# Kernel tuning notes

Measured on AMD Instinct MI355X. Metric: run time of the kernel, lower is better.

The kernel has to match this reference:

```python
import jax, jax.numpy as jnp
import numpy as np

V = 5000      # output_class_dim
E = 512       # embed_dim
F = 512       # 2 * listener_hidden_dim
H = 512       # speller_hidden_dim
HEADS = 4
HD = F // HEADS  # 128
STEPS = 64    # max_label_len
B, T = 32, 1024


def setup_inputs() -> dict:
    key = jax.random.key(0)
    ks = jax.random.split(key, 10)
    s = 0.05
    return {
        "listener_feature": jax.random.normal(ks[0], (B, T, F), jnp.float32),
        "embedding": jax.random.normal(ks[1], (V, E), jnp.float32) * s,
        # LSTM cell (single layer, torch gate order i,f,g,o)
        "W_ih": jax.random.normal(ks[2], (4 * H, E + F), jnp.float32) * s,
        "W_hh": jax.random.normal(ks[3], (4 * H, H), jnp.float32) * s,
        "b_ih": jax.random.normal(ks[4], (4 * H,), jnp.float32) * s,
        "b_hh": jax.random.normal(ks[5], (4 * H,), jnp.float32) * s,
        # predict_hid: Linear(2H -> 512)
        "Wp": jax.random.normal(ks[6], (512, 2 * H), jnp.float32) * s,
        "bp": jax.random.normal(ks[7], (512,), jnp.float32) * s,
        # character_distribution: Linear(512 -> V)
        "Wc": jax.random.normal(ks[8], (V, 512), jnp.float32) * s,
        "bc": jax.random.normal(ks[9], (V,), jnp.float32) * s,
    }


def _decode(listener_feature, embedding, W_ih, W_hh, b_ih, b_hh, Wp, bp, Wc, bc):
    b = listener_feature.shape[0]
    lf_heads = listener_feature.reshape(b, T, HEADS, HD)  # [B,T,h,d]

    def lstm_cell(x, h, c):
        gates = x @ W_ih.T + h @ W_hh.T + (b_ih + b_hh)
        i, f, g, o = jnp.split(gates, 4, axis=-1)
        c_new = jax.nn.sigmoid(f) * c + jax.nn.sigmoid(i) * jnp.tanh(g)
        h_new = jax.nn.sigmoid(o) * jnp.tanh(c_new)
        return h_new, c_new

    def step(carry, _):
        h, c, rnn_in = carry
        h, c = lstm_cell(rnn_in, h, c)                       # rnn_output = h [B,H]
        ds = h.reshape(b, HEADS, HD)                          # decoder state per head
        energy = jnp.einsum('bhd,bthd->bht', ds, lf_heads)    # dot attention
        scores = jax.nn.softmax(energy, axis=-1)              # [B,h,T]
        context = jnp.einsum('bht,bthd->bhd', scores, lf_heads).reshape(b, F)
        concat = jnp.concatenate([h, context], axis=-1)       # [B,2H]
        hid = jnp.maximum(concat @ Wp.T + bp, 0.0)            # ReLU MLP
        raw_pred = jax.nn.log_softmax(hid @ Wc.T + bc, axis=-1)
        # greedy feedback (teacher_force_rate = 0 since ground_truth is None)
        tok = jnp.argmax(raw_pred, axis=-1)                   # [B]
        rnn_in_next = jnp.concatenate([embedding[tok], context], axis=-1)
        return (h, c, rnn_in_next), (raw_pred, scores[:, -1, :])

    h0 = jnp.zeros((b, H), listener_feature.dtype)
    c0 = jnp.zeros((b, H), listener_feature.dtype)
    # initial input: embedding of token 0, concat first listener frame
    emb0 = jnp.broadcast_to(embedding[0], (b, E))
    rnn_in0 = jnp.concatenate([emb0, listener_feature[:, 0, :]], axis=-1)

    _, (raw_pred_seq, attn_seq) = jax.lax.scan(step, (h0, c0, rnn_in0), None, length=STEPS)
    return raw_pred_seq, attn_seq  # [S,B,V], [S,B,T] (last head, as in original)


def reference(listener_feature, embedding, W_ih, W_hh, b_ih, b_hh, Wp, bp, Wc, bc):
    return _decode(listener_feature, embedding, W_ih, W_hh, b_ih, b_hh, Wp, bp, Wc, bc)
```

## Files before the change

### kernel.cpp

```cpp
#include <hip/hip_runtime.h>
#include <math.h>
#include <stdint.h>


#define NB 512
#define NT 256

constexpr int Tv = 1024, Vv = 5000, STEPS = 64;

constexpr int MCNT = 0;
constexpr int GEN  = 16;
constexpr int GCNT = 64;
constexpr int GFLG = 1024;
constexpr int ACNT = 2048;
constexpr int LCNT = 2560;
constexpr int WSU  = 4096;

constexpr int XH   = 0;
constexpr int HB   = XH + 32*1024;
constexpr int HID  = HB + 2*32*512;
constexpr int PART = HID + 32*512;
constexpr int E3   = PART + 32*4*16*130;
constexpr int PM   = E3 + 32*1024;
constexpr int PSUM = PM + 32*256;
constexpr int PIDX = PSUM + 32*256;
constexpr int MLS  = PIDX + 32*256;

__device__ __forceinline__ float sigm(float x) { return 1.f / (1.f + expf(-x)); }

__device__ __forceinline__ float ld4(const float* p) {
  return __hip_atomic_load(const_cast<float*>(p), __ATOMIC_RELAXED, __HIP_MEMORY_SCOPE_AGENT);
}
__device__ __forceinline__ void st4(float* p, float v) {
  __hip_atomic_store(p, v, __ATOMIC_RELAXED, __HIP_MEMORY_SCOPE_AGENT);
}
__device__ __forceinline__ float2 ld8(const float* p) {
  unsigned long long u = __hip_atomic_load(
      reinterpret_cast<unsigned long long*>(const_cast<float*>(p)),
      __ATOMIC_RELAXED, __HIP_MEMORY_SCOPE_AGENT);
  union { unsigned long long u; float2 f; } c; c.u = u; return c.f;
}
__device__ __forceinline__ void st8(float* p, float2 v) {
  union { float2 f; unsigned long long u; } c; c.f = v;
  __hip_atomic_store(reinterpret_cast<unsigned long long*>(p), c.u,
                     __ATOMIC_RELAXED, __HIP_MEMORY_SCOPE_AGENT);
}
__device__ __forceinline__ int ld4i(const int* p) {
  return (int)__hip_atomic_load(reinterpret_cast<unsigned*>(const_cast<int*>(p)),
                                __ATOMIC_RELAXED, __HIP_MEMORY_SCOPE_AGENT);
}
__device__ __forceinline__ void st4i(int* p, int v) {
  __hip_atomic_store(reinterpret_cast<unsigned*>(p), (unsigned)v,
                     __ATOMIC_RELAXED, __HIP_MEMORY_SCOPE_AGENT);
}
__device__ __forceinline__ unsigned ld_rlx(unsigned* p) {
  return __hip_atomic_load(p, __ATOMIC_RELAXED, __HIP_MEMORY_SCOPE_AGENT);
}
__device__ __forceinline__ void st_rlx(unsigned* p, unsigned v) {
  __hip_atomic_store(p, v, __ATOMIC_RELAXED, __HIP_MEMORY_SCOPE_AGENT);
}
__device__ __forceinline__ unsigned add_rlx(unsigned* p, unsigned v) {
  return __hip_atomic_fetch_add(p, v, __ATOMIC_RELAXED, __HIP_MEMORY_SCOPE_AGENT);
}

__device__ __forceinline__ void gsync(unsigned* wsu, int blk, int tid, unsigned& myGen) {
  __syncthreads();
  if (tid == 0) {
    const unsigned target = ++myGen;
    const int grp = blk >> 4;
    unsigned o = add_rlx(&wsu[GCNT + grp*16], 1u);
    if (o == target*16u - 1u) {
      unsigned o2 = add_rlx(&wsu[MCNT], 1u);
      if (o2 == target*32u - 1u) st_rlx(&wsu[GEN], target);
    }
    if ((blk & 15) == 0) {
      while (ld_rlx(&wsu[GEN]) != target) __builtin_amdgcn_s_sleep(2);
      st_rlx(&wsu[GFLG + grp*32], target);
    } else {
      while (ld_rlx(&wsu[GFLG + grp*32]) != target) __builtin_amdgcn_s_sleep(2);
    }
  }
  __syncthreads();
}

__global__ void speller_init(const float* __restrict__ LF, const float* __restrict__ Emb,
                             float* __restrict__ wsf, unsigned* __restrict__ wsu) {
  int b = blockIdx.x;
  for (int i = threadIdx.x; i < 512; i += NT) {
    st4(wsf + XH + b*1024 + i,       Emb[i]);
    st4(wsf + XH + b*1024 + 512 + i, LF[(size_t)b*Tv*512 + i]);
    st4(wsf + HB + b*512 + i,        0.f);
  }
  if (b == 0) for (int i = threadIdx.x; i < WSU; i += NT) st_rlx(wsu + i, 0u);
}

struct LdsA { float Wg[8][1536]; float gb[8]; };
struct LdsB { float Wc[20][512]; float Wp[2][1024]; float bcl[20]; float bpl[2]; };
union  LdsU { LdsA a; LdsB b; };

__device__ __forceinline__ void gate_accum_A(float acc[8][2], const float* __restrict__ wsf,
                                             const float (&Wg)[8][1536],
                                             int ks, int b0, int hbuf) {
#pragma unroll 2
  for (int q = 0; q < 8; ++q) {
    const int k4 = 512 + (q*16 + ks)*4;
    float2 xa[2], xb[2];
#pragma unroll
    for (int i = 0; i < 2; ++i) {
      const float* p = wsf + XH + (size_t)(b0+i)*1024 + k4;
      xa[i] = ld8(p); xb[i] = ld8(p + 2);
    }
#pragma unroll
    for (int r = 0; r < 8; ++r) {
      float4 wv = *(const float4*)(&Wg[r][k4]);
#pragma unroll
      for (int i = 0; i < 2; ++i)
        acc[r][i] += wv.x*xa[i].x + wv.y*xa[i].y + wv.z*xb[i].x + wv.w*xb[i].y;
    }
  }
#pragma unroll 2
  for (int q = 0; q < 8; ++q) {
    const int k4 = (q*16 + ks)*4;
    float2 xa[2], xb[2];
#pragma unroll
    for (int i = 0; i < 2; ++i) {
      const float* p = wsf + HB + hbuf*16384 + (size_t)(b0+i)*512 + k4;
      xa[i] = ld8(p); xb[i] = ld8(p + 2);
    }
#pragma unroll
    for (int r = 0; r < 8; ++r) {
      float4 wv = *(const float4*)(&Wg[r][1024 + k4]);
#pragma unroll
      for (int i = 0; i < 2; ++i)
        acc[r][i] += wv.x*xa[i].x + wv.y*xa[i].y + wv.z*xb[i].x + wv.w*xb[i].y;
    }
  }
}

__launch_bounds__(NT, 2)
__global__ void speller_main(const float* __restrict__ LF, const float* __restrict__ Emb,
                             const float* __restrict__ Wih, const float* __restrict__ Whh,
                             const float* __restrict__ bih, const float* __restrict__ bhh,
                             const float* __restrict__ Wp,  const float* __restrict__ bp,
                             const float* __restrict__ Wc,  const float* __restrict__ bc,
                             float* __restrict__ out, unsigned* __restrict__ wsu,
                             float* __restrict__ wsf) {
  const int blk = blockIdx.x, tid = threadIdx.x;
  unsigned myGen = 0;
  __shared__ LdsU lds;
  __shared__ float scr[784];
  __shared__ int  sint[300];

  const int ab = blk >> 4, atc = blk & 15;
  const int aw = tid >> 6, aln = tid & 63;

  float4 lfr[32];
  {
    const float4* src = (const float4*)(LF +
        (((size_t)ab*Tv + atc*64 + aln)*512 + aw*128));
#pragma unroll
    for (int q = 0; q < 32; ++q) lfr[q] = src[q];
  }

  if (blk < 256) {
    const int u0 = blk * 2;
    for (int idx = tid; idx < 8*1536; idx += NT) {
      int r = idx / 1536, k = idx - r*1536;
      int g = r >> 1, uu = r & 1;
      int row = g*512 + u0 + uu;
      lds.a.Wg[r][k] = (k < 1024) ? Wih[(size_t)row*1024 + k]
                                  : Whh[(size_t)row*512 + (k-1024)];
    }
    if (tid < 8) {
      int g = tid >> 1, uu = tid & 1, row = g*512 + u0 + uu;
      lds.a.gb[tid] = bih[row] + bhh[row];
    }
  } else {
    const int blk2 = blk - 256, v0 = blk2*20, rp0 = blk2*2;
    if (v0 < Vv) {
      for (int idx = tid; idx < 20*512; idx += NT) {
        int vi = idx >> 9, k = idx & 511;
        lds.b.Wc[vi][k] = Wc[(size_t)(v0+vi)*512 + k];
      }
      if (tid < 20) lds.b.bcl[tid] = bc[v0+tid];
    }
    for (int idx = tid; idx < 2048; idx += NT) {
      int r = idx >> 10, k = idx & 1023;
      lds.b.Wp[r][k] = Wp[(size_t)(rp0+r)*1024 + k];
    }
    if (tid < 2) lds.b.bpl[tid] = bp[rp0+tid];
  }
  __syncthreads();

  float acc[8][2];
  float c_reg[2][2];
#pragma unroll
  for (int uu = 0; uu < 2; ++uu)
#pragma unroll
    for (int i = 0; i < 2; ++i) c_reg[uu][i] = 0.f;
  float lgv[20];

  if (blk < 256) {
    const int ks = tid & 15, b0 = (tid >> 4) * 2;
#pragma unroll
    for (int r = 0; r < 8; ++r)
#pragma unroll
      for (int i = 0; i < 2; ++i) acc[r][i] = 0.f;
    gate_accum_A(acc, wsf, lds.a.Wg, ks, b0, 0);
  }

#pragma unroll 1
  for (int s = 0; s < STEPS; ++s) {
    const int wbuf = (s + 1) & 1;

    if (blk < 256) {
      const int u0 = blk * 2;
      const int ks = tid & 15, b0 = (tid >> 4) * 2;
#pragma unroll 2
      for (int q = 0; q < 8; ++q) {
        const int k4 = (q*16 + ks)*4;
        float2 xa[2], xb[2];
#pragma unroll
        for (int i = 0; i < 2; ++i) {
          const float* p = wsf + XH + (size_t)(b0+i)*1024 + k4;
          xa[i] = ld8(p); xb[i] = ld8(p + 2);
        }
#pragma unroll
        for (int r = 0; r < 8; ++r) {
          float4 wv = *(const float4*)(&lds.a.Wg[r][k4]);
#pragma unroll
          for (int i = 0; i < 2; ++i)
            acc[r][i] += wv.x*xa[i].x + wv.y*xa[i].y + wv.z*xb[i].x + wv.w*xb[i].y;
        }
      }
#pragma unroll
      for (int r = 0; r < 8; ++r)
#pragma unroll
        for (int i = 0; i < 2; ++i) {
          float v = acc[r][i];
          v += __shfl_xor(v, 8); v += __shfl_xor(v, 4);
          v += __shfl_xor(v, 2); v += __shfl_xor(v, 1);
          acc[r][i] = v + lds.a.gb[r];
        }
      float hnew[2][2];
#pragma unroll
      for (int uu = 0; uu < 2; ++uu)
#pragma unroll
        for (int i = 0; i < 2; ++i) {
          float cn = sigm(acc[2+uu][i]) * c_reg[uu][i]
                   + sigm(acc[uu][i]) * tanhf(acc[4+uu][i]);
          c_reg[uu][i] = cn;
          hnew[uu][i] = sigm(acc[6+uu][i]) * tanhf(cn);
        }
      if (ks == 0) {
#pragma unroll
        for (int i = 0; i < 2; ++i)
          st8(wsf + HB + wbuf*16384 + (size_t)(b0+i)*512 + u0,
              make_float2(hnew[0][i], hnew[1][i]));
      }
    } else if (s > 0) {
      const int blk2 = blk - 256;
      if (blk2 < 250) {
        const int v0 = blk2 * 20, bb = tid >> 3, ks = tid & 7;
        if (ks == 0) {
          float2 ml = ld8(wsf + MLS + 2*bb);
          float sub = ml.x + ml.y;
#pragma unroll
          for (int vi = 0; vi < 20; ++vi)
            out[(size_t)(s-1)*160000 + (size_t)bb*5000 + v0 + vi] = lgv[vi] - sub;
        }
      }
    }
    gsync(wsu, blk, tid, myGen);

    {
      float* hs = scr;
      {
        float2 hv = ld8(wsf + HB + wbuf*16384 + (size_t)ab*512 + tid*2);
        hs[tid*2] = hv.x; hs[tid*2+1] = hv.y;
      }
      __syncthreads();
      float e = 0.f;
      {
        const float4* hp = (const float4*)(hs + aw*128);
#pragma unroll
        for (int q = 0; q < 32; ++q) {
          float4 f = lfr[q], hh = hp[q];
          e += f.x*hh.x + f.y*hh.y + f.z*hh.z + f.w*hh.w;
        }
      }
      float m = e;
#pragma unroll
      for (int off = 32; off; off >>= 1) m = fmaxf(m, __shfl_xor(m, off));
      float p = expf(e - m);
      float l = p;
#pragma unroll
      for (int off = 32; off; off >>= 1) l += __shfl_xor(l, off);
      if (aw == 3) st4(wsf + E3 + (size_t)ab*1024 + atc*64 + aln, e);
      float* pr = wsf + PART + (size_t)((ab*4 + aw)*16 + atc)*130;
#pragma unroll
      for (int ch = 0; ch < 2; ++ch) {
        float c[64];
#pragma unroll
        for (int q = 0; q < 16; ++q) {
          float4 f = lfr[ch*16 + q];
          c[4*q+0] = p*f.x; c[4*q+1] = p*f.y; c[4*q+2] = p*f.z; c[4*q+3] = p*f.w;
        }
#pragma unroll
        for (int o = 32; o >= 1; o >>= 1) {
#pragma unroll
          for (int j = 0; j < 32; ++j) {
            if (j < o) {
              float keep = (aln & o) ? c[j + o] : c[j];
              float send = (aln & o) ? c[j] : c[j + o];
              c[j] = keep + __shfl_xor(send, o);
            }
          }
        }
        st4(pr + 2 + ch*64 + aln, c[0]);
      }
      if (aln == 0) st8(pr, make_float2(m, l));
      __syncthreads();
      if (tid == 0) {
        unsigned old = add_rlx(&wsu[ACNT + ab*16], 1u);
        sint[0] = (old == (unsigned)(s*16 + 15));
      }
      __syncthreads();
      if (sint[0]) {
        const int w2 = tid >> 6, ln2 = tid & 63;
        const float* pb = wsf + PART + (size_t)(ab*4 + w2)*16*130;
        float M = -1e30f;
        float mv[16], lv[16];
#pragma unroll
        for (int i = 0; i < 16; ++i) { float2 t = ld8(pb + i*130); mv[i] = t.x; lv[i] = t.y; M = fmaxf(M, t.x); }
        float L = 0.f;
        float sc[16];
#pragma unroll
        for (int i = 0; i < 16; ++i) { sc[i] = expf(mv[i] - M); L += lv[i] * sc[i]; }
        float cc0 = 0.f, cc1 = 0.f;
#pragma unroll
        for (int i = 0; i < 16; ++i) {
          float2 cx = ld8(pb + i*130 + 2 + 2*ln2);
          cc0 += sc[i]*cx.x; cc1 += sc[i]*cx.y;
        }
        float invL = 1.f / L;
        st8(wsf + XH + (size_t)ab*1024 + 512 + w2*128 + 2*ln2,
            make_float2(cc0*invL, cc1*invL));
        if (ln2 == 0) { scr[768 + w2*2] = M; scr[769 + w2*2] = L; }
        __syncthreads();
        float M3 = scr[768 + 6], iL3 = 1.f / scr[768 + 7];
        for (int i = tid; i < 1024; i += NT)
          out[(size_t)10240000 + ((size_t)(s*32 + ab))*1024 + i] =
              expf(ld4(wsf + E3 + (size_t)ab*1024 + i) - M3) * iL3;
      }
    }
    gsync(wsu, blk, tid, myGen);

    if (blk >= 256) {
      const int blk2 = blk - 256, rp0 = blk2*2;
      const int bb = tid & 31, ks = tid >> 5;
      const float* xr = (ks < 4) ? (wsf + HB + wbuf*16384 + (size_t)bb*512 + ks*128)
                                 : (wsf + XH + (size_t)bb*1024 + (ks-4)*128 + 512);
      const int kb = ks * 128;
      const float4* w0 = (const float4*)(&lds.b.Wp[0][kb]);
      const float4* w1 = (const float4*)(&lds.b.Wp[1][kb]);
      float a0 = 0.f, a1 = 0.f;
#pragma unroll 8
      for (int q = 0; q < 32; ++q) {
        float2 xva = ld8(xr + q*4), xvb = ld8(xr + q*4 + 2);
        float4 wv0 = w0[q], wv1 = w1[q];
        a0 += wv0.x*xva.x + wv0.y*xva.y + wv0.z*xvb.x + wv0.w*xvb.y;
        a1 += wv1.x*xva.x + wv1.y*xva.y + wv1.z*xvb.x + wv1.w*xvb.y;
      }
      scr[ks*32 + bb] = a0; scr[256 + ks*32 + bb] = a1;
      __syncthreads();
      if (tid < 64) {
        int r = tid >> 5, b2 = tid & 31;
        float ssum = 0.f;
#pragma unroll
        for (int j = 0; j < 8; ++j) ssum += scr[r*256 + j*32 + b2];
        ssum += lds.b.bpl[r];
        st4(wsf + HID + (size_t)b2*512 + rp0 + r, fmaxf(ssum, 0.f));
      }
      __syncthreads();
    } else if (s < 63) {
      const int ks = tid & 15, b0 = (tid >> 4) * 2;
#pragma unroll
      for (int r = 0; r < 8; ++r)
#pragma unroll
        for (int i = 0; i < 2; ++i) acc[r][i] = 0.f;
      gate_accum_A(acc, wsf, lds.a.Wg, ks, b0, wbuf);
    }
    gsync(wsu, blk, tid, myGen);

    if (blk >= 256) {
      const int blk2 = blk - 256;
      if (blk2 < 250) {
        const int v0 = blk2 * 20;
        const int bb = tid >> 3, ks = tid & 7;
#pragma unroll
        for (int vi = 0; vi < 20; ++vi) lgv[vi] = 0.f;
        const float* hb = wsf + HID + (size_t)bb*512;
#pragma unroll 1
        for (int half = 0; half < 2; ++half) {
          float4 xr[8];
#pragma unroll
          for (int q = 0; q < 8; ++q) {
            const float* p = hb + ((half*8 + q)*8 + ks)*4;
            float2 a = ld8(p), b2v = ld8(p + 2);
            xr[q] = make_float4(a.x, a.y, b2v.x, b2v.y);
          }
#pragma unroll
          for (int vi = 0; vi < 20; ++vi) {
            float a = 0.f;
#pragma unroll
            for (int q = 0; q < 8; ++q) {
              float4 wv = *(const float4*)(&lds.b.Wc[vi][((half*8 + q)*8 + ks)*4]);
              a += wv.x*xr[q].x + wv.y*xr[q].y + wv.z*xr[q].z + wv.w*xr[q].w;
            }
            lgv[vi] += a;
          }
        }
#pragma unroll
        for (int vi = 0; vi < 20; ++vi) {
          float a = lgv[vi];
          a += __shfl_xor(a, 1); a += __shfl_xor(a, 2); a += __shfl_xor(a, 4);
          lgv[vi] = a + lds.b.bcl[vi];
        }
        float mych = lgv[0]; int ami = 0;
#pragma unroll
        for (int vi = 1; vi < 20; ++vi)
          if (lgv[vi] > mych) { mych = lgv[vi]; ami = vi; }
        float sume = 0.f;
#pragma unroll
        for (int vi = 0; vi < 20; ++vi) sume += expf(lgv[vi] - mych);
        if (ks == 0) {
          st4(wsf + PM + bb*256 + blk2, mych);
          st4(wsf + PSUM + bb*256 + blk2, sume);
          st4i((int*)(wsf + PIDX) + bb*256 + blk2, v0 + ami);
        }
      }
      __syncthreads();
      if (tid == 0 && blk2 < 250) add_rlx(&wsu[LCNT], 1u);
      if (blk2 < 32) {
        const int b2 = blk2;
        if (tid == 0) {
          while (ld_rlx(&wsu[LCNT]) < (unsigned)((s + 1) * 250))
            __builtin_amdgcn_s_sleep(2);
        }
        __syncthreads();
        float mv = -1e30f, sv = 0.f; int iv = 0x7fffffff;
        if (tid < 250) {
          mv = ld4(wsf + PM + b2*256 + tid);
          sv = ld4(wsf + PSUM + b2*256 + tid);
          iv = ld4i((const int*)(wsf + PIDX) + b2*256 + tid);
        }
        scr[tid] = mv; sint[40 + tid] = iv;
        __syncthreads();
        for (int off = 128; off; off >>= 1) {
          if (tid < off) {
            float m2 = scr[tid + off]; int i2 = sint[40 + tid + off];
            if (m2 > scr[tid] || (m2 == scr[tid] && i2 < sint[40 + tid])) {
              scr[tid] = m2; sint[40 + tid] = i2;
            }
          }
          __syncthreads();
        }
        float M = scr[0]; int tok = sint[40];
        __syncthreads();
        scr[tid] = sv * expf(mv - M);
        __syncthreads();
        for (int off = 128; off; off >>= 1) {
          if (tid < off) scr[tid] += scr[tid + off];
          __syncthreads();
        }
        if (tid == 0) st8(wsf + MLS + 2*b2, make_float2(M, logf(scr[0])));
        for (int i = tid; i < 256; i += NT) {
          const float2* er = (const float2*)(Emb + (size_t)tok*512);
          st8(wsf + XH + (size_t)b2*1024 + 2*i, er[i]);
        }
      }
    }
    gsync(wsu, blk, tid, myGen);
  }

  if (blk >= 256) {
    const int blk2 = blk - 256;
    if (blk2 < 250) {
      const int v0 = blk2 * 20, bb = tid >> 3, ks = tid & 7;
      if (ks == 0) {
        float2 ml = ld8(wsf + MLS + 2*bb);
        float sub = ml.x + ml.y;
#pragma unroll
        for (int vi = 0; vi < 20; ++vi)
          out[(size_t)63*160000 + (size_t)bb*5000 + v0 + vi] = lgv[vi] - sub;
      }
    }
  }
}

extern "C" void kernel_launch(void* const* d_in, const int* in_sizes, int n_in,
                              void* d_out, int out_size, void* d_ws, size_t ws_size,
                              hipStream_t stream) {
  (void)in_sizes; (void)n_in; (void)out_size; (void)ws_size;
  const float* LF  = (const float*)d_in[0];
  const float* Emb = (const float*)d_in[1];
  const float* Wih = (const float*)d_in[2];
  const float* Whh = (const float*)d_in[3];
  const float* bih = (const float*)d_in[4];
  const float* bhh = (const float*)d_in[5];
  const float* Wp  = (const float*)d_in[6];
  const float* bp  = (const float*)d_in[7];
  const float* Wc  = (const float*)d_in[8];
  const float* bc  = (const float*)d_in[9];
  float* out = (float*)d_out;
  unsigned* wsu = (unsigned*)d_ws;
  float* wsf = (float*)d_ws + WSU;

  speller_init<<<32, NT, 0, stream>>>(LF, Emb, wsf, wsu);
  speller_main<<<NB, NT, 0, stream>>>(LF, Emb, Wih, Whh, bih, bhh, Wp, bp, Wc, bc,
                                      out, wsu, wsf);
}
```

Baseline: 6.665 ms.

## Fuse predict_hid projection into LSTM gate accumulation blocks

The ReLU projection (Wp) moves from the logits blocks into the gate blocks. Each gate block now holds two extra Wp rows in LDS and accumulates them in the same pass over context and h that already feeds the gate preactivations, then reduces with wave shuffles. This removes a separate reload of h/context and its LDS reduction in the second group of blocks. In exchange it adds LDS use and work per gate block, and the gate pass now also runs on the last step. Spin-wait sleep intervals are also raised from 2 to 8.

```diff
diff --git a/kernel.cpp b/kernel.cpp
--- a/kernel.cpp
+++ b/kernel.cpp
@@ -31,23 +31,23 @@
 __device__ __forceinline__ float ld4(const float* p) {
   return __hip_atomic_load(const_cast<float*>(p), __ATOMIC_RELAXED, __HIP_MEMORY_SCOPE_AGENT);
 }
-__device__ __forceinline__ void st4(float* p, float v) {
-  __hip_atomic_store(p, v, __ATOMIC_RELAXED, __HIP_MEMORY_SCOPE_AGENT);
-}
 __device__ __forceinline__ float2 ld8(const float* p) {
   unsigned long long u = __hip_atomic_load(
       reinterpret_cast<unsigned long long*>(const_cast<float*>(p)),
       __ATOMIC_RELAXED, __HIP_MEMORY_SCOPE_AGENT);
   union { unsigned long long u; float2 f; } c; c.u = u; return c.f;
 }
+__device__ __forceinline__ int ld4i(const int* p) {
+  return (int)__hip_atomic_load(reinterpret_cast<unsigned*>(const_cast<int*>(p)),
+                                __ATOMIC_RELAXED, __HIP_MEMORY_SCOPE_AGENT);
+}
+__device__ __forceinline__ void st4(float* p, float v) {
+  __hip_atomic_store(p, v, __ATOMIC_RELAXED, __HIP_MEMORY_SCOPE_AGENT);
+}
 __device__ __forceinline__ void st8(float* p, float2 v) {
   union { float2 f; unsigned long long u; } c; c.f = v;
   __hip_atomic_store(reinterpret_cast<unsigned long long*>(p), c.u,
                      __ATOMIC_RELAXED, __HIP_MEMORY_SCOPE_AGENT);
-}
-__device__ __forceinline__ int ld4i(const int* p) {
-  return (int)__hip_atomic_load(reinterpret_cast<unsigned*>(const_cast<int*>(p)),
-                                __ATOMIC_RELAXED, __HIP_MEMORY_SCOPE_AGENT);
 }
 __device__ __forceinline__ void st4i(int* p, int v) {
   __hip_atomic_store(reinterpret_cast<unsigned*>(p), (unsigned)v,
@@ -74,10 +74,10 @@
       if (o2 == target*32u - 1u) st_rlx(&wsu[GEN], target);
     }
     if ((blk & 15) == 0) {
-      while (ld_rlx(&wsu[GEN]) != target) __builtin_amdgcn_s_sleep(2);
+      while (ld_rlx(&wsu[GEN]) != target) __builtin_amdgcn_s_sleep(8);
       st_rlx(&wsu[GFLG + grp*32], target);
     } else {
-      while (ld_rlx(&wsu[GFLG + grp*32]) != target) __builtin_amdgcn_s_sleep(2);
+      while (ld_rlx(&wsu[GFLG + grp*32]) != target) __builtin_amdgcn_s_sleep(8);
     }
   }
   __syncthreads();
@@ -94,12 +94,14 @@
   if (b == 0) for (int i = threadIdx.x; i < WSU; i += NT) st_rlx(wsu + i, 0u);
 }
 
-struct LdsA { float Wg[8][1536]; float gb[8]; };
-struct LdsB { float Wc[20][512]; float Wp[2][1024]; float bcl[20]; float bpl[2]; };
+struct LdsA { float Wg[8][1536]; float Wpg[2][1536]; float gb[8]; float bpg[2]; };
+struct LdsB { float Wc[20][512]; float bcl[20]; };
 union  LdsU { LdsA a; LdsB b; };
 
-__device__ __forceinline__ void gate_accum_A(float acc[8][2], const float* __restrict__ wsf,
+__device__ __forceinline__ void gate_accum_A(float acc[8][2], float accW[2][2],
+                                             const float* __restrict__ wsf,
                                              const float (&Wg)[8][1536],
+                                             const float (&Wpg)[2][1536],
                                              int ks, int b0, int hbuf) {
 #pragma unroll 2
   for (int q = 0; q < 8; ++q) {
@@ -117,6 +119,13 @@
       for (int i = 0; i < 2; ++i)
         acc[r][i] += wv.x*xa[i].x + wv.y*xa[i].y + wv.z*xb[i].x + wv.w*xb[i].y;
     }
+#pragma unroll
+    for (int r = 0; r < 2; ++r) {
+      float4 wv = *(const float4*)(&Wpg[r][k4]);
+#pragma unroll
+      for (int i = 0; i < 2; ++i)
+        accW[r][i] += wv.x*xa[i].x + wv.y*xa[i].y + wv.z*xb[i].x + wv.w*xb[i].y;
+    }
   }
 #pragma unroll 2
   for (int q = 0; q < 8; ++q) {
@@ -133,6 +142,13 @@
 #pragma unroll
       for (int i = 0; i < 2; ++i)
         acc[r][i] += wv.x*xa[i].x + wv.y*xa[i].y + wv.z*xb[i].x + wv.w*xb[i].y;
+    }
+#pragma unroll
+    for (int r = 0; r < 2; ++r) {
+      float4 wv = *(const float4*)(&Wpg[r][1024 + k4]);
+#pragma unroll
+      for (int i = 0; i < 2; ++i)
+        accW[r][i] += wv.x*xa[i].x + wv.y*xa[i].y + wv.z*xb[i].x + wv.w*xb[i].y;
     }
   }
 }
@@ -171,12 +187,20 @@
       lds.a.Wg[r][k] = (k < 1024) ? Wih[(size_t)row*1024 + k]
                                   : Whh[(size_t)row*512 + (k-1024)];
     }
+    for (int idx = tid; idx < 2*1536; idx += NT) {
+      int r = idx / 1536, k = idx - r*1536;
+      float v = 0.f;
+      if (k >= 512) v = (k < 1024) ? Wp[(size_t)(u0+r)*1024 + k]
+                                   : Wp[(size_t)(u0+r)*1024 + (k-1024)];
+      lds.a.Wpg[r][k] = v;
+    }
     if (tid < 8) {
       int g = tid >> 1, uu = tid & 1, row = g*512 + u0 + uu;
       lds.a.gb[tid] = bih[row] + bhh[row];
     }
+    if (tid < 2) lds.a.bpg[tid] = bp[u0 + tid];
   } else {
-    const int blk2 = blk - 256, v0 = blk2*20, rp0 = blk2*2;
+    const int blk2 = blk - 256, v0 = blk2*20;
     if (v0 < Vv) {
       for (int idx = tid; idx < 20*512; idx += NT) {
         int vi = idx >> 9, k = idx & 511;
@@ -184,15 +208,11 @@
       }
       if (tid < 20) lds.b.bcl[tid] = bc[v0+tid];
     }
-    for (int idx = tid; idx < 2048; idx += NT) {
-      int r = idx >> 10, k = idx & 1023;
-      lds.b.Wp[r][k] = Wp[(size_t)(rp0+r)*1024 + k];
-    }
-    if (tid < 2) lds.b.bpl[tid] = bp[rp0+tid];
   }
   __syncthreads();
 
   float acc[8][2];
+  float accW[2][2];
   float c_reg[2][2];
 #pragma unroll
   for (int uu = 0; uu < 2; ++uu)
@@ -206,7 +226,11 @@
     for (int r = 0; r < 8; ++r)
 #pragma unroll
       for (int i = 0; i < 2; ++i) acc[r][i] = 0.f;
-    gate_accum_A(acc, wsf, lds.a.Wg, ks, b0, 0);
+#pragma unroll
+    for (int r = 0; r < 2; ++r)
+#pragma unroll
+      for (int i = 0; i < 2; ++i) accW[r][i] = 0.f;
+    gate_accum_A(acc, accW, wsf, lds.a.Wg, lds.a.Wpg, ks, b0, 0);
   }
 
 #pragma unroll 1
@@ -356,40 +380,32 @@
     }
     gsync(wsu, blk, tid, myGen);
 
-    if (blk >= 256) {
-      const int blk2 = blk - 256, rp0 = blk2*2;
-      const int bb = tid & 31, ks = tid >> 5;
-      const float* xr = (ks < 4) ? (wsf + HB + wbuf*16384 + (size_t)bb*512 + ks*128)
-                                 : (wsf + XH + (size_t)bb*1024 + (ks-4)*128 + 512);
-      const int kb = ks * 128;
-      const float4* w0 = (const float4*)(&lds.b.Wp[0][kb]);
-      const float4* w1 = (const float4*)(&lds.b.Wp[1][kb]);
-      float a0 = 0.f, a1 = 0.f;
-#pragma unroll 8
-      for (int q = 0; q < 32; ++q) {
-        float2 xva = ld8(xr + q*4), xvb = ld8(xr + q*4 + 2);
-        float4 wv0 = w0[q], wv1 = w1[q];
-        a0 += wv0.x*xva.x + wv0.y*xva.y + wv0.z*xvb.x + wv0.w*xvb.y;
-        a1 += wv1.x*xva.x + wv1.y*xva.y + wv1.z*xvb.x + wv1.w*xvb.y;
-      }
-      scr[ks*32 + bb] = a0; scr[256 + ks*32 + bb] = a1;
-      __syncthreads();
-      if (tid < 64) {
-        int r = tid >> 5, b2 = tid & 31;
-        float ssum = 0.f;
-#pragma unroll
-        for (int j = 0; j < 8; ++j) ssum += scr[r*256 + j*32 + b2];
-        ssum += lds.b.bpl[r];
-        st4(wsf + HID + (size_t)b2*512 + rp0 + r, fmaxf(ssum, 0.f));
-      }
-      __syncthreads();
-    } else if (s < 63) {
+    if (blk < 256) {
       const int ks = tid & 15, b0 = (tid >> 4) * 2;
 #pragma unroll
       for (int r = 0; r < 8; ++r)
 #pragma unroll
         for (int i = 0; i < 2; ++i) acc[r][i] = 0.f;
-      gate_accum_A(acc, wsf, lds.a.Wg, ks, b0, wbuf);
+#pragma unroll
+      for (int r = 0; r < 2; ++r)
+#pragma unroll
+        for (int i = 0; i < 2; ++i) accW[r][i] = 0.f;
+      gate_accum_A(acc, accW, wsf, lds.a.Wg, lds.a.Wpg, ks, b0, wbuf);
+#pragma unroll
+      for (int r = 0; r < 2; ++r)
+#pragma unroll
+        for (int i = 0; i < 2; ++i) {
+          float v = accW[r][i];
+          v += __shfl_xor(v, 8); v += __shfl_xor(v, 4);
+          v += __shfl_xor(v, 2); v += __shfl_xor(v, 1);
+          accW[r][i] = v + lds.a.bpg[r];
+        }
+      if (ks == 0) {
+#pragma unroll
+        for (int i = 0; i < 2; ++i)
+          st8(wsf + HID + (size_t)(b0+i)*512 + blk*2,
+              make_float2(fmaxf(accW[0][i], 0.f), fmaxf(accW[1][i], 0.f)));
+      }
     }
     gsync(wsu, blk, tid, myGen);
 
@@ -446,7 +462,7 @@
         const int b2 = blk2;
         if (tid == 0) {
           while (ld_rlx(&wsu[LCNT]) < (unsigned)((s + 1) * 250))
-            __builtin_amdgcn_s_sleep(2);
+            __builtin_amdgcn_s_sleep(8);
         }
         __syncthreads();
         float mv = -1e30f, sv = 0.f; int iv = 0x7fffffff;
```

Result: faster. 5.857 ms (-12.1%).
